# Kernel tuning notes

Measured on AMD Instinct MI355X. Metric: run time of the kernel, lower is better.

The kernel has to match this reference:

```python
import jax, jax.numpy as jnp
import numpy as np
import math

SIGMA_DATA = 0.5
SIGMA_MIN = 0.002
SIGMA_MAX = 80.0
B = 32768
STATE = 256
ACT = 64
TD = 16
E = 16
H = 256  # moe hidden = gate_dim = output_dim = hidden_dim//4
IN = STATE + ACT + TD  # 336
TOP_K = 4


def mish(x):
    return x * jnp.tanh(jax.nn.softplus(x))


def setup_inputs() -> dict:
    key = jax.random.key(0)
    ks = jax.random.split(key, 20)
    def xavier(k, shape):
        fan_in, fan_out = shape[-2], shape[-1]
        lim = math.sqrt(6.0 / (fan_in + fan_out))
        return jax.random.uniform(k, shape, jnp.float32, -lim, lim)
    inp = {
        "x": jax.random.normal(ks[0], (B, ACT), jnp.float32),
        "sigma": jax.random.uniform(ks[1], (B,), jnp.float32) * (SIGMA_MAX - SIGMA_MIN) + SIGMA_MIN,
        "state": jax.random.normal(ks[2], (B, STATE), jnp.float32),
        # time MLP: Linear(16,32), Mish, Linear(32,16)
        "tW1": xavier(ks[3], (TD, 2 * TD)), "tb1": jnp.zeros((2 * TD,), jnp.float32),
        "tW2": xavier(ks[4], (2 * TD, TD)), "tb2": jnp.zeros((TD,), jnp.float32),
        # gate: Linear(IN, H), ReLU, (dropout eval), Linear(H, E)
        "gW1": xavier(ks[5], (IN, H)), "gb1": jnp.zeros((H,), jnp.float32),
        "gW2": xavier(ks[6], (H, E)), "gb2": jnp.zeros((E,), jnp.float32),
        # 16 stacked expert MLPs: IN->H->H->H with Mish after each Linear
        "eW1": xavier(ks[7], (E, IN, H)), "eb1": jnp.zeros((E, H), jnp.float32),
        "eW2": xavier(ks[8], (E, H, H)), "eb2": jnp.zeros((E, H), jnp.float32),
        "eW3": xavier(ks[9], (E, H, H)), "eb3": jnp.zeros((E, H), jnp.float32),
        # final layer: Linear(H, ACT)
        "fW": xavier(ks[10], (H, ACT)), "fb": jnp.zeros((ACT,), jnp.float32),
    }
    return inp


def reference(x, sigma, state, tW1, tb1, tW2, tb2, gW1, gb1, gW2, gb2,
              eW1, eb1, eW2, eb2, eW3, eb3, fW, fb):
    # --- consistency-model scalings (boundary condition) ---
    c_skip = SIGMA_DATA ** 2 / ((sigma - SIGMA_MIN) ** 2 + SIGMA_DATA ** 2)
    c_out = (sigma - SIGMA_MIN) * SIGMA_DATA * jax.lax.rsqrt(sigma ** 2 + SIGMA_DATA ** 2)
    c_in = jax.lax.rsqrt(sigma ** 2 + SIGMA_DATA ** 2)
    rescaled_t = 1000.0 * 0.25 * jnp.log(sigma + 1e-44)

    x_in = c_in[:, None] * x

    # --- sinusoidal time embedding (dim=16) + time MLP ---
    half = TD // 2
    freqs = jnp.exp(jnp.arange(half, dtype=jnp.float32) * (-math.log(10000.0) / (half - 1)))
    ang = rescaled_t[:, None] * freqs[None, :]           # [B, 8]
    pe = jnp.concatenate([jnp.sin(ang), jnp.cos(ang)], axis=-1)  # [B, 16]
    t = mish(pe @ tW1 + tb1) @ tW2 + tb2                 # [B, 16]

    inp = jnp.concatenate([x_in, t, state], axis=1)      # [B, 336]

    # --- gate (eval mode: dropout off) ---
    g = jax.nn.relu(inp @ gW1 + gb1) @ gW2 + gb2         # [B, E]
    gate_scores = jax.nn.softmax(g, axis=1)
    top_k_scores, top_k_idx = jax.lax.top_k(gate_scores, TOP_K)  # [B, K]

    # --- run ALL experts densely (as the original does) ---
    h = mish(jnp.einsum('bi,eih->beh', inp, eW1) + eb1)  # [B, E, H]
    h = mish(jnp.einsum('beh,ehk->bek', h, eW2) + eb2)
    expert_out = mish(jnp.einsum('beh,eho->beo', h, eW3) + eb3)  # [B, E, H]

    # --- gather top-k, scale by normalized gate scores, combine ---
    sel = jnp.take_along_axis(expert_out, top_k_idx[:, :, None], axis=1)  # [B, K, H]
    scaled = sel * top_k_scores[:, :, None]
    scaled = scaled / (jnp.sum(top_k_scores, axis=1, keepdims=True)[:, :, None] + 1e-9)
    combined = jnp.sum(scaled, axis=1)                   # [B, H]

    # --- auxiliary loss ---
    one_hot = jax.nn.one_hot(top_k_idx, E, dtype=jnp.float32)  # [B, K, E]
    expert_load = jnp.sum(one_hot, axis=(0, 1)) / (x.shape[0] + 1e-9)
    load_balancing_loss = jnp.var(expert_load, ddof=1)   # torch .var() is unbiased
    entropy = -jnp.mean(jnp.sum(gate_scores * jnp.log(gate_scores + 1e-9), axis=1))
    aux_loss = load_balancing_loss + entropy

    model_out = combined @ fW + fb                       # [B, ACT]
    denoised = c_out[:, None] * model_out + c_skip[:, None] * x
    denoised = jnp.clip(denoised, -1.0, 1.0)             # clip_denoised=True
    return denoised, aux_loss
```

## Files before the change

kernel.cpp:

```cpp
#include <hip/hip_runtime.h>
#include <math.h>

#define BN 32768
#define INDP 352
#define HD 256
#define AD 64
#define EN 16
#define TM 64
#define STOT (BN * 4)
#define LDP 256
#define GRID_E 2072
#define CHUNK_E 259

typedef __attribute__((ext_vector_type(8))) short s8v;
typedef __attribute__((ext_vector_type(4))) float f4v;
typedef unsigned short u16;

__device__ __forceinline__ u16 f2bf(float x) {
  unsigned u = __float_as_uint(x);
  return (u16)((u + 0x7fffu + ((u >> 16) & 1u)) >> 16);
}
__device__ __forceinline__ float bf2f(u16 h) { return __uint_as_float(((unsigned)h) << 16); }
__device__ __forceinline__ float rcpf(float a) { float r; asm("v_rcp_f32 %0, %1" : "=v"(r) : "v"(a)); return r; }
__device__ __forceinline__ float mishf(float x) {
  float xc = fminf(x, 30.f);
  float u = __expf(xc);
  float w = fmaf(u, u, u + u);
  return x * w * rcpf(w + 2.f);
}
__device__ __forceinline__ f4v mfma16(s8v a, s8v b, f4v c) {
  return __builtin_amdgcn_mfma_f32_16x16x32_bf16(a, b, c, 0, 0, 0);
}
__device__ __forceinline__ void pack8(const u16* q, u16* d) {
  uint4 u;
  u.x = q[0] | ((unsigned)q[1] << 16); u.y = q[2] | ((unsigned)q[3] << 16);
  u.z = q[4] | ((unsigned)q[5] << 16); u.w = q[6] | ((unsigned)q[7] << 16);
  *(uint4*)d = u;
}

__global__ void k_init(float* __restrict__ out, int* __restrict__ counts,
                       int* __restrict__ cursor, float* __restrict__ ent) {
  int i = blockIdx.x * 256 + threadIdx.x;
  if (i < BN * AD) out[i] = 0.f;
  if (i < 16) { counts[i] = 0; cursor[i] = 0; }
  if (i == 16) *ent = 0.f;
}

__global__ void k_prep(const float* __restrict__ src, u16* __restrict__ dst,
                       int Ksrc, int Spad, int NT, int N,
                       long sStride, long dStride, int NP, int total) {
  int idx = blockIdx.x * 256 + threadIdx.x;
  if (idx >= total) return;
  int l = idx & 63;
  int t = idx >> 6;
  int nt = t % NT; t /= NT;
  int s = t % Spad; t /= Spad;
  int m = t;
  const float* sp = src + (size_t)m * sStride;
  int n = nt * 16 + (l & 15);
  int kb = s * 32 + (l >> 4) * 8;
  u16 q0[8], q1[8], q2[8];
  #pragma unroll
  for (int i = 0; i < 8; ++i) {
    int k = kb + i;
    float v = (k < Ksrc) ? sp[(size_t)k * N + n] : 0.f;
    u16 a = f2bf(v); float r1 = v - bf2f(a);
    u16 b = f2bf(r1); float r2 = r1 - bf2f(b);
    q0[i] = a; q1[i] = b; q2[i] = f2bf(r2);
  }
  u16* d = dst + (size_t)m * dStride + (size_t)((s * NT + nt) * NP) * 512 + l * 8;
  pack8(q0, d);
  pack8(q1, d + 512);
  if (NP == 3) pack8(q2, d + 1024);
}

__global__ void k_time_inp(const float* __restrict__ x, const float* __restrict__ sigma,
                           const float* __restrict__ state,
                           const float* __restrict__ tW1, const float* __restrict__ tb1,
                           const float* __restrict__ tW2, const float* __restrict__ tb2,
                           u16* __restrict__ p0, u16* __restrict__ p1, u16* __restrict__ p2) {
  const int wv = threadIdx.x >> 6;
  const int lane = threadIdx.x & 63;
  const int row = blockIdx.x * 4 + wv;
  const float sg = sigma[row];
  const float rt = 250.0f * logf(sg + 1e-44f);
  float pe = 0.f;
  if (lane < 16) {
    int j = lane & 7;
    float f = expf(-1.3157629102823121f * (float)j);
    float ang = rt * f;
    pe = (lane < 8) ? sinf(ang) : cosf(ang);
  }
  float h1;
  {
    float acc = 0.f;
    int j = lane & 31;
    #pragma unroll
    for (int i = 0; i < 16; ++i) {
      float p = __shfl(pe, i, 64);
      acc = fmaf(p, tW1[i * 32 + j], acc);
    }
    acc += tb1[j];
    float sp = log1pf(expf(acc));
    h1 = acc * tanhf(sp);
  }
  float t2;
  {
    float acc = 0.f;
    int j = lane & 15;
    #pragma unroll
    for (int i = 0; i < 32; ++i) {
      float h = __shfl(h1, i, 64);
      acc = fmaf(h, tW2[i * 16 + j], acc);
    }
    t2 = acc + tb2[j];
  }
  const float c_in = rsqrtf(sg * sg + 0.25f);
  u16* r0 = p0 + (size_t)row * INDP;
  u16* r1 = p1 + (size_t)row * INDP;
  u16* r2 = p2 + (size_t)row * INDP;
  auto wsplit = [&](int c, float v) {
    u16 a = f2bf(v); float ra = v - bf2f(a);
    u16 b = f2bf(ra); float rb = ra - bf2f(b);
    r0[c] = a; r1[c] = b; r2[c] = f2bf(rb);
  };
  wsplit(lane, c_in * x[row * 64 + lane]);
  if (lane < 16) wsplit(64 + lane, t2);
  #pragma unroll
  for (int r = 0; r < 4; ++r)
    wsplit(80 + r * 64 + lane, state[(size_t)row * 256 + r * 64 + lane]);
  if (lane < 16) { r0[336 + lane] = 0; r1[336 + lane] = 0; r2[336 + lane] = 0; }
}

__global__ __launch_bounds__(256) void k_gate(
    const u16* __restrict__ p0, const u16* __restrict__ p1, const u16* __restrict__ p2,
    const u16* __restrict__ gW1b, const float* __restrict__ gb1,
    const float* __restrict__ gW2, const float* __restrict__ gb2,
    int* __restrict__ topk_idx, float* __restrict__ topk_w,
    int* __restrict__ counts, float* __restrict__ ent_sum) {
  __shared__ float sH[TM * 257];
  __shared__ float sB2[256 * 16];
  __shared__ float sLog[TM * 16];
  __shared__ int scnt[16];
  const int tid = threadIdx.x;
  const int l = tid & 63, w = tid >> 6;
  const int g = l >> 4, r16 = l & 15;
  const int row0 = blockIdx.x * TM;
  if (tid < 16) scnt[tid] = 0;

  f4v acc[4][4];
  #pragma unroll
  for (int i = 0; i < 4; ++i)
    #pragma unroll
    for (int j = 0; j < 4; ++j) acc[i][j] = (f4v){0.f, 0.f, 0.f, 0.f};

  for (int s = 0; s < 11; ++s) {
    s8v a0[4], a1[4], a2[4], b0[4], b1[4], b2[4];
    #pragma unroll
    for (int mt = 0; mt < 4; ++mt) {
      size_t off = (size_t)(row0 + mt * 16 + r16) * INDP + s * 32 + g * 8;
      a0[mt] = *(const s8v*)(p0 + off);
      a1[mt] = *(const s8v*)(p1 + off);
      a2[mt] = *(const s8v*)(p2 + off);
    }
    #pragma unroll
    for (int j = 0; j < 4; ++j) {
      const u16* pb = gW1b + (size_t)((s * 16 + w * 4 + j) * 3) * 512 + l * 8;
      b0[j] = *(const s8v*)pb;
      b1[j] = *(const s8v*)(pb + 512);
      b2[j] = *(const s8v*)(pb + 1024);
    }
    #pragma unroll
    for (int mt = 0; mt < 4; ++mt)
      #pragma unroll
      for (int j = 0; j < 4; ++j) {
        acc[mt][j] = mfma16(a0[mt], b0[j], acc[mt][j]);
        acc[mt][j] = mfma16(a0[mt], b1[j], acc[mt][j]);
        acc[mt][j] = mfma16(a1[mt], b0[j], acc[mt][j]);
        acc[mt][j] = mfma16(a1[mt], b1[j], acc[mt][j]);
        acc[mt][j] = mfma16(a0[mt], b2[j], acc[mt][j]);
        acc[mt][j] = mfma16(a2[mt], b0[j], acc[mt][j]);
      }
  }
  float bj[4];
  #pragma unroll
  for (int j = 0; j < 4; ++j) bj[j] = gb1[w * 64 + j * 16 + r16];
  #pragma unroll
  for (int mt = 0; mt < 4; ++mt)
    #pragma unroll
    for (int j = 0; j < 4; ++j)
      #pragma unroll
      for (int r = 0; r < 4; ++r) {
        int row = mt * 16 + g * 4 + r;
        sH[row * 257 + w * 64 + j * 16 + r16] = fmaxf(acc[mt][j][r] + bj[j], 0.f);
      }
  #pragma unroll
  for (int it = 0; it < 4; ++it) {
    int idx = tid + it * 256;
    *(float4*)&sB2[idx * 4] = *(const float4*)(gW2 + (size_t)idx * 4);
  }
  __syncthreads();
  {
    const int rr = tid >> 2, q = tid & 3;
    float g0 = 0.f, g1 = 0.f, g2 = 0.f, g3 = 0.f;
    for (int k = 0; k < 256; ++k) {
      float a = sH[rr * 257 + k];
      float4 bv = *(const float4*)&sB2[k * 16 + q * 4];
      g0 = fmaf(a, bv.x, g0); g1 = fmaf(a, bv.y, g1);
      g2 = fmaf(a, bv.z, g2); g3 = fmaf(a, bv.w, g3);
    }
    sLog[rr * 16 + q * 4 + 0] = g0 + gb2[q * 4 + 0];
    sLog[rr * 16 + q * 4 + 1] = g1 + gb2[q * 4 + 1];
    sLog[rr * 16 + q * 4 + 2] = g2 + gb2[q * 4 + 2];
    sLog[rr * 16 + q * 4 + 3] = g3 + gb2[q * 4 + 3];
  }
  __syncthreads();
  float entc = 0.f;
  if (tid < 64) {
    const int row = row0 + tid;
    float gx[16], mx = -1e30f;
    #pragma unroll
    for (int e = 0; e < 16; ++e) { gx[e] = sLog[tid * 16 + e]; mx = fmaxf(mx, gx[e]); }
    float p[16], s = 0.f;
    #pragma unroll
    for (int e = 0; e < 16; ++e) { p[e] = expf(gx[e] - mx); s += p[e]; }
    const float inv = 1.f / s;
    #pragma unroll
    for (int e = 0; e < 16; ++e) {
      float pr = p[e] * inv;
      entc -= pr * logf(pr + 1e-9f);
    }
    int idxs[4]; float scs[4];
    unsigned used = 0;
    float wsum = 1e-9f;
    #pragma unroll
    for (int k = 0; k < 4; ++k) {
      int be = 0; float bv = -1.f;
      #pragma unroll
      for (int e = 0; e < 16; ++e) {
        float pr = p[e] * inv;
        if (!((used >> e) & 1u) && pr > bv) { bv = pr; be = e; }
      }
      used |= (1u << be);
      idxs[k] = be; scs[k] = bv;
      wsum += bv;
    }
    #pragma unroll
    for (int k = 0; k < 4; ++k) {
      topk_idx[row * 4 + k] = idxs[k];
      topk_w[row * 4 + k] = scs[k] / wsum;
      atomicAdd(&scnt[idxs[k]], 1);
    }
    #pragma unroll
    for (int off = 32; off > 0; off >>= 1) entc += __shfl_down(entc, off, 64);
  }
  __syncthreads();
  if (tid == 0) atomicAdd(ent_sum, entc);
  if (tid < 16 && scnt[tid] > 0) atomicAdd(&counts[tid], scnt[tid]);
}

__global__ void k_aux(const int* __restrict__ counts, const float* __restrict__ ent_sum,
                      int* __restrict__ offsets, int* __restrict__ tbk,
                      float* __restrict__ aux_out) {
  if (threadIdx.x == 0) {
    int off = 0, t = 0;
    float load[16], mean = 0.f;
    for (int e = 0; e < 16; ++e) {
      offsets[e] = off; tbk[e] = t;
      int c = counts[e];
      off += c;
      t += (c + TM - 1) / TM;
      load[e] = (float)c / (32768.0f + 1e-9f);
      mean += load[e];
    }
    offsets[16] = off; tbk[16] = t;
    mean *= (1.f / 16.f);
    float var = 0.f;
    for (int e = 0; e < 16; ++e) { float d = load[e] - mean; var += d * d; }
    var *= (1.f / 15.f);
    *aux_out = var + ent_sum[0] * (1.0f / 32768.0f);
  }
}

__global__ void k_scatter(const int* __restrict__ topk_idx, const float* __restrict__ topk_w,
                          const int* __restrict__ offsets, int* __restrict__ cursor,
                          int* __restrict__ slot_row, float* __restrict__ slot_w) {
  __shared__ int cnt[16];
  __shared__ int base[16];
  const int tid = threadIdx.x;
  if (tid < 16) cnt[tid] = 0;
  __syncthreads();
  const int row = blockIdx.x * 256 + tid;
  int e4[4]; float w4[4]; int lp[4];
  #pragma unroll
  for (int k = 0; k < 4; ++k) {
    e4[k] = topk_idx[row * 4 + k];
    w4[k] = topk_w[row * 4 + k];
    lp[k] = atomicAdd(&cnt[e4[k]], 1);
  }
  __syncthreads();
  if (tid < 16) base[tid] = atomicAdd(&cursor[tid], cnt[tid]);
  __syncthreads();
  #pragma unroll
  for (int k = 0; k < 4; ++k) {
    int s = offsets[e4[k]] + base[e4[k]] + lp[k];
    slot_row[s] = row;
    slot_w[s] = w4[k];
  }
}

__global__ __launch_bounds__(512, 4) void k_expert(
    const u16* __restrict__ inpHi, const u16* __restrict__ inpLo,
    const u16* __restrict__ eW1b, const float* __restrict__ eb1,
    const u16* __restrict__ eW2b, const float* __restrict__ eb2,
    const u16* __restrict__ eW3b, const float* __restrict__ eb3,
    const u16* __restrict__ fWb,
    const int* __restrict__ offsets, const int* __restrict__ counts,
    const int* __restrict__ tbk, const int* __restrict__ slot_row,
    const float* __restrict__ slot_w, float* __restrict__ out) {
  __shared__ __align__(16) u16 sHi[TM * LDP];
  __shared__ __align__(16) u16 sLo[TM * LDP];
  __shared__ int sRows[TM];
  __shared__ float sWv[TM];

  const int bid = (blockIdx.x & 7) * CHUNK_E + (blockIdx.x >> 3);
  if (bid >= tbk[16]) return;
  int e = 0;
  #pragma unroll
  for (int i = 1; i < 16; ++i)
    if (bid >= tbk[i]) e = i;
  const int tile = bid - tbk[e];
  const int cnt = counts[e];
  const int s0 = offsets[e] + tile * TM;
  const int nr = min(TM, cnt - tile * TM);
  const int tid = threadIdx.x;
  const int l = tid & 63;
  const int w8 = tid >> 6;
  const int wm = w8 >> 2;
  const int wn = w8 & 3;
  const int g = l >> 4, r16 = l & 15;
  const int swz = (r16 & 7) << 3;

  if (tid < TM) {
    sRows[tid] = (tid < nr) ? slot_row[s0 + tid] : slot_row[s0];
    sWv[tid] = (tid < nr) ? slot_w[s0 + tid] : 0.f;
  }
  __syncthreads();

  size_t rbase[2];
  #pragma unroll
  for (int mt = 0; mt < 2; ++mt)
    rbase[mt] = (size_t)sRows[(wm * 2 + mt) * 16 + r16] * INDP;

  f4v acc[2][4];
  #pragma unroll
  for (int i = 0; i < 2; ++i)
    #pragma unroll
    for (int j = 0; j < 4; ++j) acc[i][j] = (f4v){0.f, 0.f, 0.f, 0.f};

  const u16* W1 = eW1b + (size_t)e * 180224;
  for (int s = 0; s < 11; ++s) {
    s8v ah[2], al[2], bh[4], bl[4];
    #pragma unroll
    for (int mt = 0; mt < 2; ++mt) {
      size_t off = rbase[mt] + s * 32 + g * 8;
      ah[mt] = *(const s8v*)(inpHi + off);
      al[mt] = *(const s8v*)(inpLo + off);
    }
    #pragma unroll
    for (int j = 0; j < 4; ++j) {
      const u16* pb = W1 + (size_t)((s * 16 + wn * 4 + j) * 2) * 512 + l * 8;
      bh[j] = *(const s8v*)pb;
      bl[j] = *(const s8v*)(pb + 512);
    }
    #pragma unroll
    for (int mt = 0; mt < 2; ++mt)
      #pragma unroll
      for (int j = 0; j < 4; ++j) {
        acc[mt][j] = mfma16(ah[mt], bh[j], acc[mt][j]);
        acc[mt][j] = mfma16(al[mt], bh[j], acc[mt][j]);
        acc[mt][j] = mfma16(ah[mt], bl[j], acc[mt][j]);
      }
  }
  {
    const float* b1 = eb1 + e * HD;
    float bj[4];
    #pragma unroll
    for (int j = 0; j < 4; ++j) bj[j] = b1[wn * 64 + j * 16 + r16];
    #pragma unroll
    for (int mt = 0; mt < 2; ++mt)
      #pragma unroll
      for (int j = 0; j < 4; ++j)
        #pragma unroll
        for (int r = 0; r < 4; ++r) {
          int row = (wm * 2 + mt) * 16 + g * 4 + r;
          int col = wn * 64 + j * 16 + r16;
          float v = mishf(acc[mt][j][r] + bj[j]);
          u16 h = f2bf(v);
          int ec = col ^ ((row & 7) << 3);
          sHi[row * LDP + ec] = h;
          sLo[row * LDP + ec] = f2bf(v - bf2f(h));
        }
  }
  __syncthreads();

  #pragma unroll 1
  for (int L = 0; L < 2; ++L) {
    const u16* Wb = (L == 0 ? eW2b : eW3b) + (size_t)e * 131072;
    const float* bb = (L == 0 ? eb2 : eb3) + e * HD;
    f4v a2[2][4];
    #pragma unroll
    for (int i = 0; i < 2; ++i)
      #pragma unroll
      for (int j = 0; j < 4; ++j) a2[i][j] = (f4v){0.f, 0.f, 0.f, 0.f};
    #pragma unroll 2
    for (int s = 0; s < 8; ++s) {
      s8v ah[2], al[2], bh[4], bl[4];
      #pragma unroll
      for (int mt = 0; mt < 2; ++mt) {
        int row = (wm * 2 + mt) * 16 + r16;
        int ec = (s * 32 + g * 8) ^ swz;
        ah[mt] = *(const s8v*)&sHi[row * LDP + ec];
        al[mt] = *(const s8v*)&sLo[row * LDP + ec];
      }
      #pragma unroll
      for (int j = 0; j < 4; ++j) {
        const u16* pb = Wb + (size_t)((s * 16 + wn * 4 + j) * 2) * 512 + l * 8;
        bh[j] = *(const s8v*)pb;
        bl[j] = *(const s8v*)(pb + 512);
      }
      #pragma unroll
      for (int mt = 0; mt < 2; ++mt)
        #pragma unroll
        for (int j = 0; j < 4; ++j) {
          a2[mt][j] = mfma16(ah[mt], bh[j], a2[mt][j]);
          a2[mt][j] = mfma16(al[mt], bh[j], a2[mt][j]);
          a2[mt][j] = mfma16(ah[mt], bl[j], a2[mt][j]);
        }
    }
    __syncthreads();
    float bj[4];
    #pragma unroll
    for (int j = 0; j < 4; ++j) bj[j] = bb[wn * 64 + j * 16 + r16];
    #pragma unroll
    for (int mt = 0; mt < 2; ++mt)
      #pragma unroll
      for (int j = 0; j < 4; ++j)
        #pragma unroll
        for (int r = 0; r < 4; ++r) {
          int row = (wm * 2 + mt) * 16 + g * 4 + r;
          int col = wn * 64 + j * 16 + r16;
          float v = mishf(a2[mt][j][r] + bj[j]);
          u16 h = f2bf(v);
          int ec = col ^ ((row & 7) << 3);
          sHi[row * LDP + ec] = h;
          sLo[row * LDP + ec] = f2bf(v - bf2f(h));
        }
    __syncthreads();
  }

  f4v a3[2];
  #pragma unroll
  for (int i = 0; i < 2; ++i) a3[i] = (f4v){0.f, 0.f, 0.f, 0.f};
  #pragma unroll 2
  for (int s = 0; s < 8; ++s) {
    s8v ah[2], al[2];
    #pragma unroll
    for (int mt = 0; mt < 2; ++mt) {
      int row = (wm * 2 + mt) * 16 + r16;
      int ec = (s * 32 + g * 8) ^ swz;
      ah[mt] = *(const s8v*)&sHi[row * LDP + ec];
      al[mt] = *(const s8v*)&sLo[row * LDP + ec];
    }
    const u16* pb = fWb + (size_t)((s * 4 + wn) * 2) * 512 + l * 8;
    s8v bh = *(const s8v*)pb;
    s8v bl = *(const s8v*)(pb + 512);
    #pragma unroll
    for (int mt = 0; mt < 2; ++mt) {
      a3[mt] = mfma16(ah[mt], bh, a3[mt]);
      a3[mt] = mfma16(al[mt], bh, a3[mt]);
      a3[mt] = mfma16(ah[mt], bl, a3[mt]);
    }
  }
  #pragma unroll
  for (int mt = 0; mt < 2; ++mt)
    #pragma unroll
    for (int r = 0; r < 4; ++r) {
      int rl = (wm * 2 + mt) * 16 + g * 4 + r;
      if (rl < nr) {
        float v = a3[mt][r] * sWv[rl];
        atomicAdd(&out[(size_t)sRows[rl] * AD + wn * 16 + r16], v);
      }
    }
}

__global__ void k_final(const float* __restrict__ x, const float* __restrict__ sigma,
                        const float* __restrict__ fb, float* __restrict__ out) {
  int i = blockIdx.x * 256 + threadIdx.x;
  if (i >= BN * AD) return;
  int row = i >> 6, c = i & 63;
  float sg = sigma[row];
  float sm = sg - 0.002f;
  float c_skip = 0.25f / (sm * sm + 0.25f);
  float c_out = sm * 0.5f * rsqrtf(sg * sg + 0.25f);
  float d = c_out * (out[i] + fb[c]) + c_skip * x[i];
  out[i] = fminf(fmaxf(d, -1.f), 1.f);
}

extern "C" void kernel_launch(void* const* d_in, const int* in_sizes, int n_in,
                              void* d_out, int out_size, void* d_ws, size_t ws_size,
                              hipStream_t stream) {
  const float* x     = (const float*)d_in[0];
  const float* sigma = (const float*)d_in[1];
  const float* state = (const float*)d_in[2];
  const float* tW1   = (const float*)d_in[3];
  const float* tb1   = (const float*)d_in[4];
  const float* tW2   = (const float*)d_in[5];
  const float* tb2   = (const float*)d_in[6];
  const float* gW1   = (const float*)d_in[7];
  const float* gb1   = (const float*)d_in[8];
  const float* gW2   = (const float*)d_in[9];
  const float* gb2   = (const float*)d_in[10];
  const float* eW1   = (const float*)d_in[11];
  const float* eb1   = (const float*)d_in[12];
  const float* eW2   = (const float*)d_in[13];
  const float* eb2   = (const float*)d_in[14];
  const float* eW3   = (const float*)d_in[15];
  const float* eb3   = (const float*)d_in[16];
  const float* fW    = (const float*)d_in[17];
  const float* fb    = (const float*)d_in[18];
  float* out = (float*)d_out;

  char* p = (char*)d_ws;
  auto alloc = [&](size_t bytes) { void* r = (void*)p; p += (bytes + 255) & ~(size_t)255; return r; };
  u16* inpHi  = (u16*)alloc((size_t)BN * INDP * 2);
  u16* inpLo  = (u16*)alloc((size_t)BN * INDP * 2);
  u16* inpMid = (u16*)alloc((size_t)BN * INDP * 2);
  u16* gW1b   = (u16*)alloc((size_t)11 * 16 * 3 * 512 * 2);
  u16* eW1b   = (u16*)alloc((size_t)16 * 180224 * 2);
  u16* eW2b   = (u16*)alloc((size_t)16 * 131072 * 2);
  u16* eW3b   = (u16*)alloc((size_t)16 * 131072 * 2);
  u16* fWb    = (u16*)alloc((size_t)32768 * 2);
  int*   topk_idx = (int*)alloc((size_t)BN * 4 * 4);
  float* topk_w   = (float*)alloc((size_t)BN * 4 * 4);
  int*   counts   = (int*)alloc(64);
  int*   cursor   = (int*)alloc(64);
  int*   offsets  = (int*)alloc(68);
  int*   tbk      = (int*)alloc(68);
  float* ent      = (float*)alloc(4);
  int*   slot_row = (int*)alloc((size_t)STOT * 4);
  float* slot_w   = (float*)alloc((size_t)STOT * 4);

  k_init<<<(BN * AD + 255) / 256, 256, 0, stream>>>(out, counts, cursor, ent);

  int tot;
  tot = 16 * 11 * 16 * 64;
  k_prep<<<(tot + 255) / 256, 256, 0, stream>>>(eW1, eW1b, 336, 11, 16, 256,
                                                (long)336 * 256, 180224, 2, tot);
  tot = 16 * 8 * 16 * 64;
  k_prep<<<(tot + 255) / 256, 256, 0, stream>>>(eW2, eW2b, 256, 8, 16, 256,
                                                (long)256 * 256, 131072, 2, tot);
  k_prep<<<(tot + 255) / 256, 256, 0, stream>>>(eW3, eW3b, 256, 8, 16, 256,
                                                (long)256 * 256, 131072, 2, tot);
  tot = 11 * 16 * 64;
  k_prep<<<(tot + 255) / 256, 256, 0, stream>>>(gW1, gW1b, 336, 11, 16, 256,
                                                0, 0, 3, tot);
  tot = 8 * 4 * 64;
  k_prep<<<(tot + 255) / 256, 256, 0, stream>>>(fW, fWb, 256, 8, 4, 64,
                                                0, 0, 2, tot);

  k_time_inp<<<BN / 4, 256, 0, stream>>>(x, sigma, state, tW1, tb1, tW2, tb2,
                                         inpHi, inpLo, inpMid);
  k_gate<<<BN / TM, 256, 0, stream>>>(inpHi, inpLo, inpMid, gW1b, gb1, gW2, gb2,
                                      topk_idx, topk_w, counts, ent);
  k_aux<<<1, 64, 0, stream>>>(counts, ent, offsets, tbk, out + (size_t)BN * AD);
  k_scatter<<<BN / 256, 256, 0, stream>>>(topk_idx, topk_w, offsets, cursor, slot_row, slot_w);
  k_expert<<<GRID_E, 512, 0, stream>>>(inpHi, inpLo, eW1b, eb1, eW2b, eb2,
                                       eW3b, eb3, fWb, offsets, counts, tbk,
                                       slot_row, slot_w, out);
  k_final<<<(BN * AD + 255) / 256, 256, 0, stream>>>(x, sigma, fb, out);
}
```

Before: 521.4 us.

## Halve row tiles to 32 and move the gate's second layer onto 3xBF16 MFMA

Row tiles for the gate and expert kernels shrink from 64 to 32 rows. The expert kernel drops to 256 threads and gets a doubled grid, and the gate kernel adds a launch-bounds occupancy hint. The gate's second linear layer moves from a scalar FP32 shared-memory loop to MFMA using a three-way bf16 split of the hidden activations in swizzled LDS, with gW2 prepacked by an extra prep launch. The aim is more blocks for occupancy and padding efficiency, plus less scalar FMA work in the gate. In exchange, each expert weight tile is reused over fewer rows, so weight traffic per row doubles.

```diff
diff --git a/kernel.cpp b/kernel.cpp
--- a/kernel.cpp
+++ b/kernel.cpp
@@ -6,11 +6,10 @@
 #define HD 256
 #define AD 64
 #define EN 16
-#define TM 64
+#define TME 32
 #define STOT (BN * 4)
-#define LDP 256
-#define GRID_E 2072
-#define CHUNK_E 259
+#define GRID_E 4112
+#define CHUNK_E 514
 
 typedef __attribute__((ext_vector_type(8))) short s8v;
 typedef __attribute__((ext_vector_type(4))) float f4v;
@@ -132,32 +131,35 @@
   if (lane < 16) { r0[336 + lane] = 0; r1[336 + lane] = 0; r2[336 + lane] = 0; }
 }
 
-__global__ __launch_bounds__(256) void k_gate(
+__global__ __launch_bounds__(256, 3) void k_gate(
     const u16* __restrict__ p0, const u16* __restrict__ p1, const u16* __restrict__ p2,
     const u16* __restrict__ gW1b, const float* __restrict__ gb1,
-    const float* __restrict__ gW2, const float* __restrict__ gb2,
+    const u16* __restrict__ gW2b, const float* __restrict__ gb2,
     int* __restrict__ topk_idx, float* __restrict__ topk_w,
     int* __restrict__ counts, float* __restrict__ ent_sum) {
-  __shared__ float sH[TM * 257];
-  __shared__ float sB2[256 * 16];
-  __shared__ float sLog[TM * 16];
+  __shared__ __align__(16) u16 sH0[TME * 256];
+  __shared__ __align__(16) u16 sH1[TME * 256];
+  __shared__ __align__(16) u16 sH2[TME * 256];
+  __shared__ float sLog[TME * 16];
   __shared__ int scnt[16];
   const int tid = threadIdx.x;
-  const int l = tid & 63, w = tid >> 6;
+  const int l = tid & 63, wn = tid >> 6;
   const int g = l >> 4, r16 = l & 15;
-  const int row0 = blockIdx.x * TM;
+  const int row0 = blockIdx.x * TME;
+  const int swz = (r16 & 7) << 3;
   if (tid < 16) scnt[tid] = 0;
 
-  f4v acc[4][4];
-  #pragma unroll
-  for (int i = 0; i < 4; ++i)
+  f4v acc[2][4];
+  #pragma unroll
+  for (int i = 0; i < 2; ++i)
     #pragma unroll
     for (int j = 0; j < 4; ++j) acc[i][j] = (f4v){0.f, 0.f, 0.f, 0.f};
 
+  #pragma unroll 2
   for (int s = 0; s < 11; ++s) {
-    s8v a0[4], a1[4], a2[4], b0[4], b1[4], b2[4];
-    #pragma unroll
-    for (int mt = 0; mt < 4; ++mt) {
+    s8v a0[2], a1[2], a2[2], b0[4], b1[4], b2[4];
+    #pragma unroll
+    for (int mt = 0; mt < 2; ++mt) {
       size_t off = (size_t)(row0 + mt * 16 + r16) * INDP + s * 32 + g * 8;
       a0[mt] = *(const s8v*)(p0 + off);
       a1[mt] = *(const s8v*)(p1 + off);
@@ -165,13 +167,13 @@
     }
     #pragma unroll
     for (int j = 0; j < 4; ++j) {
-      const u16* pb = gW1b + (size_t)((s * 16 + w * 4 + j) * 3) * 512 + l * 8;
+      const u16* pb = gW1b + (size_t)((s * 16 + wn * 4 + j) * 3) * 512 + l * 8;
       b0[j] = *(const s8v*)pb;
       b1[j] = *(const s8v*)(pb + 512);
       b2[j] = *(const s8v*)(pb + 1024);
     }
     #pragma unroll
-    for (int mt = 0; mt < 4; ++mt)
+    for (int mt = 0; mt < 2; ++mt)
       #pragma unroll
       for (int j = 0; j < 4; ++j) {
         acc[mt][j] = mfma16(a0[mt], b0[j], acc[mt][j]);
@@ -182,41 +184,61 @@
         acc[mt][j] = mfma16(a2[mt], b0[j], acc[mt][j]);
       }
   }
-  float bj[4];
-  #pragma unroll
-  for (int j = 0; j < 4; ++j) bj[j] = gb1[w * 64 + j * 16 + r16];
-  #pragma unroll
-  for (int mt = 0; mt < 4; ++mt)
-    #pragma unroll
-    for (int j = 0; j < 4; ++j)
+  #pragma unroll
+  for (int mt = 0; mt < 2; ++mt)
+    #pragma unroll
+    for (int j = 0; j < 4; ++j) {
+      float bj = gb1[wn * 64 + j * 16 + r16];
       #pragma unroll
       for (int r = 0; r < 4; ++r) {
         int row = mt * 16 + g * 4 + r;
-        sH[row * 257 + w * 64 + j * 16 + r16] = fmaxf(acc[mt][j][r] + bj[j], 0.f);
-      }
-  #pragma unroll
-  for (int it = 0; it < 4; ++it) {
-    int idx = tid + it * 256;
-    *(float4*)&sB2[idx * 4] = *(const float4*)(gW2 + (size_t)idx * 4);
-  }
-  __syncthreads();
-  {
-    const int rr = tid >> 2, q = tid & 3;
-    float g0 = 0.f, g1 = 0.f, g2 = 0.f, g3 = 0.f;
-    for (int k = 0; k < 256; ++k) {
-      float a = sH[rr * 257 + k];
-      float4 bv = *(const float4*)&sB2[k * 16 + q * 4];
-      g0 = fmaf(a, bv.x, g0); g1 = fmaf(a, bv.y, g1);
-      g2 = fmaf(a, bv.z, g2); g3 = fmaf(a, bv.w, g3);
-    }
-    sLog[rr * 16 + q * 4 + 0] = g0 + gb2[q * 4 + 0];
-    sLog[rr * 16 + q * 4 + 1] = g1 + gb2[q * 4 + 1];
-    sLog[rr * 16 + q * 4 + 2] = g2 + gb2[q * 4 + 2];
-    sLog[rr * 16 + q * 4 + 3] = g3 + gb2[q * 4 + 3];
-  }
-  __syncthreads();
+        int col = wn * 64 + j * 16 + r16;
+        float v = fmaxf(acc[mt][j][r] + bj, 0.f);
+        u16 h0 = f2bf(v); float ra = v - bf2f(h0);
+        u16 h1 = f2bf(ra); float rb = ra - bf2f(h1);
+        int ec = col ^ ((row & 7) << 3);
+        sH0[row * 256 + ec] = h0;
+        sH1[row * 256 + ec] = h1;
+        sH2[row * 256 + ec] = f2bf(rb);
+      }
+    }
+  __syncthreads();
+
+  f4v l2[2];
+  l2[0] = (f4v){0.f, 0.f, 0.f, 0.f};
+  l2[1] = (f4v){0.f, 0.f, 0.f, 0.f};
+  #pragma unroll
+  for (int s = 0; s < 8; ++s) {
+    const u16* pb = gW2b + (size_t)(s * 3) * 512 + l * 8;
+    s8v b0 = *(const s8v*)pb;
+    s8v b1 = *(const s8v*)(pb + 512);
+    s8v b2 = *(const s8v*)(pb + 1024);
+    #pragma unroll
+    for (int mt = 0; mt < 2; ++mt) {
+      int row = mt * 16 + r16;
+      int ec = (s * 32 + g * 8) ^ swz;
+      s8v a0 = *(const s8v*)&sH0[row * 256 + ec];
+      s8v a1 = *(const s8v*)&sH1[row * 256 + ec];
+      s8v a2 = *(const s8v*)&sH2[row * 256 + ec];
+      l2[mt] = mfma16(a0, b0, l2[mt]);
+      l2[mt] = mfma16(a0, b1, l2[mt]);
+      l2[mt] = mfma16(a1, b0, l2[mt]);
+      l2[mt] = mfma16(a1, b1, l2[mt]);
+      l2[mt] = mfma16(a0, b2, l2[mt]);
+      l2[mt] = mfma16(a2, b0, l2[mt]);
+    }
+  }
+  if (wn == 0) {
+    #pragma unroll
+    for (int mt = 0; mt < 2; ++mt)
+      #pragma unroll
+      for (int r = 0; r < 4; ++r)
+        sLog[(mt * 16 + g * 4 + r) * 16 + r16] = l2[mt][r] + gb2[r16];
+  }
+  __syncthreads();
+
   float entc = 0.f;
-  if (tid < 64) {
+  if (tid < TME) {
     const int row = row0 + tid;
     float gx[16], mx = -1e30f;
     #pragma unroll
@@ -251,11 +273,13 @@
       topk_w[row * 4 + k] = scs[k] / wsum;
       atomicAdd(&scnt[idxs[k]], 1);
     }
+  }
+  if (tid < 64) {
     #pragma unroll
     for (int off = 32; off > 0; off >>= 1) entc += __shfl_down(entc, off, 64);
   }
-  __syncthreads();
   if (tid == 0) atomicAdd(ent_sum, entc);
+  __syncthreads();
   if (tid < 16 && scnt[tid] > 0) atomicAdd(&counts[tid], scnt[tid]);
 }
 
@@ -269,7 +293,7 @@
       offsets[e] = off; tbk[e] = t;
       int c = counts[e];
       off += c;
-      t += (c + TM - 1) / TM;
+      t += (c + TME - 1) / TME;
       load[e] = (float)c / (32768.0f + 1e-9f);
       mean += load[e];
     }
@@ -309,7 +333,7 @@
   }
 }
 
-__global__ __launch_bounds__(512, 4) void k_expert(
+__global__ __launch_bounds__(256, 4) void k_expert(
     const u16* __restrict__ inpHi, const u16* __restrict__ inpLo,
     const u16* __restrict__ eW1b, const float* __restrict__ eb1,
     const u16* __restrict__ eW2b, const float* __restrict__ eb2,
@@ -318,10 +342,10 @@
     const int* __restrict__ offsets, const int* __restrict__ counts,
     const int* __restrict__ tbk, const int* __restrict__ slot_row,
     const float* __restrict__ slot_w, float* __restrict__ out) {
-  __shared__ __align__(16) u16 sHi[TM * LDP];
-  __shared__ __align__(16) u16 sLo[TM * LDP];
-  __shared__ int sRows[TM];
-  __shared__ float sWv[TM];
+  __shared__ __align__(16) u16 sHi[TME * 256];
+  __shared__ __align__(16) u16 sLo[TME * 256];
+  __shared__ int sRows[TME];
+  __shared__ float sWv[TME];
 
   const int bid = (blockIdx.x & 7) * CHUNK_E + (blockIdx.x >> 3);
   if (bid >= tbk[16]) return;
@@ -331,17 +355,15 @@
     if (bid >= tbk[i]) e = i;
   const int tile = bid - tbk[e];
   const int cnt = counts[e];
-  const int s0 = offsets[e] + tile * TM;
-  const int nr = min(TM, cnt - tile * TM);
+  const int s0 = offsets[e] + tile * TME;
+  const int nr = min(TME, cnt - tile * TME);
   const int tid = threadIdx.x;
   const int l = tid & 63;
-  const int w8 = tid >> 6;
-  const int wm = w8 >> 2;
-  const int wn = w8 & 3;
+  const int wn = tid >> 6;
   const int g = l >> 4, r16 = l & 15;
   const int swz = (r16 & 7) << 3;
 
-  if (tid < TM) {
+  if (tid < TME) {
     sRows[tid] = (tid < nr) ? slot_row[s0 + tid] : slot_row[s0];
     sWv[tid] = (tid < nr) ? slot_w[s0 + tid] : 0.f;
   }
@@ -350,7 +372,7 @@
   size_t rbase[2];
   #pragma unroll
   for (int mt = 0; mt < 2; ++mt)
-    rbase[mt] = (size_t)sRows[(wm * 2 + mt) * 16 + r16] * INDP;
+    rbase[mt] = (size_t)sRows[mt * 16 + r16] * INDP;
 
   f4v acc[2][4];
   #pragma unroll
@@ -359,6 +381,7 @@
     for (int j = 0; j < 4; ++j) acc[i][j] = (f4v){0.f, 0.f, 0.f, 0.f};
 
   const u16* W1 = eW1b + (size_t)e * 180224;
+  #pragma unroll 2
   for (int s = 0; s < 11; ++s) {
     s8v ah[2], al[2], bh[4], bl[4];
     #pragma unroll
@@ -384,23 +407,22 @@
   }
   {
     const float* b1 = eb1 + e * HD;
-    float bj[4];
-    #pragma unroll
-    for (int j = 0; j < 4; ++j) bj[j] = b1[wn * 64 + j * 16 + r16];
     #pragma unroll
     for (int mt = 0; mt < 2; ++mt)
       #pragma unroll
-      for (int j = 0; j < 4; ++j)
+      for (int j = 0; j < 4; ++j) {
+        float bj = b1[wn * 64 + j * 16 + r16];
         #pragma unroll
         for (int r = 0; r < 4; ++r) {
-          int row = (wm * 2 + mt) * 16 + g * 4 + r;
+          int row = mt * 16 + g * 4 + r;
           int col = wn * 64 + j * 16 + r16;
-          float v = mishf(acc[mt][j][r] + bj[j]);
+          float v = mishf(acc[mt][j][r] + bj);
           u16 h = f2bf(v);
           int ec = col ^ ((row & 7) << 3);
-          sHi[row * LDP + ec] = h;
-          sLo[row * LDP + ec] = f2bf(v - bf2f(h));
+          sHi[row * 256 + ec] = h;
+          sLo[row * 256 + ec] = f2bf(v - bf2f(h));
         }
+      }
   }
   __syncthreads();
 
@@ -418,10 +440,10 @@
       s8v ah[2], al[2], bh[4], bl[4];
       #pragma unroll
       for (int mt = 0; mt < 2; ++mt) {
-        int row = (wm * 2 + mt) * 16 + r16;
+        int row = mt * 16 + r16;
         int ec = (s * 32 + g * 8) ^ swz;
-        ah[mt] = *(const s8v*)&sHi[row * LDP + ec];
-        al[mt] = *(const s8v*)&sLo[row * LDP + ec];
+        ah[mt] = *(const s8v*)&sHi[row * 256 + ec];
+        al[mt] = *(const s8v*)&sLo[row * 256 + ec];
       }
       #pragma unroll
       for (int j = 0; j < 4; ++j) {
@@ -439,38 +461,37 @@
         }
     }
     __syncthreads();
-    float bj[4];
-    #pragma unroll
-    for (int j = 0; j < 4; ++j) bj[j] = bb[wn * 64 + j * 16 + r16];
     #pragma unroll
     for (int mt = 0; mt < 2; ++mt)
       #pragma unroll
-      for (int j = 0; j < 4; ++j)
+      for (int j = 0; j < 4; ++j) {
+        float bj = bb[wn * 64 + j * 16 + r16];
         #pragma unroll
         for (int r = 0; r < 4; ++r) {
-          int row = (wm * 2 + mt) * 16 + g * 4 + r;
+          int row = mt * 16 + g * 4 + r;
           int col = wn * 64 + j * 16 + r16;
-          float v = mishf(a2[mt][j][r] + bj[j]);
+          float v = mishf(a2[mt][j][r] + bj);
           u16 h = f2bf(v);
           int ec = col ^ ((row & 7) << 3);
-          sHi[row * LDP + ec] = h;
-          sLo[row * LDP + ec] = f2bf(v - bf2f(h));
+          sHi[row * 256 + ec] = h;
+          sLo[row * 256 + ec] = f2bf(v - bf2f(h));
         }
+      }
     __syncthreads();
   }
 
   f4v a3[2];
-  #pragma unroll
-  for (int i = 0; i < 2; ++i) a3[i] = (f4v){0.f, 0.f, 0.f, 0.f};
+  a3[0] = (f4v){0.f, 0.f, 0.f, 0.f};
+  a3[1] = (f4v){0.f, 0.f, 0.f, 0.f};
   #pragma unroll 2
   for (int s = 0; s < 8; ++s) {
     s8v ah[2], al[2];
     #pragma unroll
     for (int mt = 0; mt < 2; ++mt) {
-      int row = (wm * 2 + mt) * 16 + r16;
+      int row = mt * 16 + r16;
       int ec = (s * 32 + g * 8) ^ swz;
-      ah[mt] = *(const s8v*)&sHi[row * LDP + ec];
-      al[mt] = *(const s8v*)&sLo[row * LDP + ec];
+      ah[mt] = *(const s8v*)&sHi[row * 256 + ec];
+      al[mt] = *(const s8v*)&sLo[row * 256 + ec];
     }
     const u16* pb = fWb + (size_t)((s * 4 + wn) * 2) * 512 + l * 8;
     s8v bh = *(const s8v*)pb;
@@ -486,7 +507,7 @@
   for (int mt = 0; mt < 2; ++mt)
     #pragma unroll
     for (int r = 0; r < 4; ++r) {
-      int rl = (wm * 2 + mt) * 16 + g * 4 + r;
+      int rl = mt * 16 + g * 4 + r;
       if (rl < nr) {
         float v = a3[mt][r] * sWv[rl];
         atomicAdd(&out[(size_t)sRows[rl] * AD + wn * 16 + r16], v);
@@ -537,6 +558,7 @@
   u16* inpLo  = (u16*)alloc((size_t)BN * INDP * 2);
   u16* inpMid = (u16*)alloc((size_t)BN * INDP * 2);
   u16* gW1b   = (u16*)alloc((size_t)11 * 16 * 3 * 512 * 2);
+  u16* gW2b   = (u16*)alloc((size_t)8 * 3 * 512 * 2);
   u16* eW1b   = (u16*)alloc((size_t)16 * 180224 * 2);
   u16* eW2b   = (u16*)alloc((size_t)16 * 131072 * 2);
   u16* eW3b   = (u16*)alloc((size_t)16 * 131072 * 2);
@@ -565,17 +587,20 @@
   tot = 11 * 16 * 64;
   k_prep<<<(tot + 255) / 256, 256, 0, stream>>>(gW1, gW1b, 336, 11, 16, 256,
                                                 0, 0, 3, tot);
+  tot = 8 * 1 * 64;
+  k_prep<<<(tot + 255) / 256, 256, 0, stream>>>(gW2, gW2b, 256, 8, 1, 16,
+                                                0, 0, 3, tot);
   tot = 8 * 4 * 64;
   k_prep<<<(tot + 255) / 256, 256, 0, stream>>>(fW, fWb, 256, 8, 4, 64,
                                                 0, 0, 2, tot);
 
   k_time_inp<<<BN / 4, 256, 0, stream>>>(x, sigma, state, tW1, tb1, tW2, tb2,
                                          inpHi, inpLo, inpMid);
-  k_gate<<<BN / TM, 256, 0, stream>>>(inpHi, inpLo, inpMid, gW1b, gb1, gW2, gb2,
-                                      topk_idx, topk_w, counts, ent);
+  k_gate<<<BN / TME, 256, 0, stream>>>(inpHi, inpLo, inpMid, gW1b, gb1, gW2b, gb2,
+                                       topk_idx, topk_w, counts, ent);
   k_aux<<<1, 64, 0, stream>>>(counts, ent, offsets, tbk, out + (size_t)BN * AD);
   k_scatter<<<BN / 256, 256, 0, stream>>>(topk_idx, topk_w, offsets, cursor, slot_row, slot_w);
-  k_expert<<<GRID_E, 512, 0, stream>>>(inpHi, inpLo, eW1b, eb1, eW2b, eb2,
+  k_expert<<<GRID_E, 256, 0, stream>>>(inpHi, inpLo, eW1b, eb1, eW2b, eb2,
                                        eW3b, eb3, fWb, offsets, counts, tbk,
                                        slot_row, slot_w, out);
   k_final<<<(BN * AD + 255) / 256, 256, 0, stream>>>(x, sigma, fb, out);
```

Measured after the change: 467.1 us. -10.4%, faster.
